# Kernel tuning notes

Hardware: AMD Instinct MI355X
Metric: run time of the kernel (lower is better)

## Reference

```python
import jax, jax.numpy as jnp
import numpy as np

B = 512
C = 256
HEADS = 16
DH = 16
SIGMA = 1e-4  # GaussianNoise(0.0001)
LEAK = 0.2


def _axial_attn(x, Wq, Wkv, Wo, bo, axis):
    # x: [B, 8, 4, 5, C]; attend along `axis`, folding other dims into batch.
    xm = jnp.moveaxis(x, axis, -2)                      # [..., T, C]
    q = xm @ Wq                                          # [..., T, C]
    kv = xm @ Wkv                                        # [..., T, 2C]
    k, v = kv[..., :C], kv[..., C:]
    hshape = q.shape[:-1] + (HEADS, DH)
    q = q.reshape(hshape)
    k = k.reshape(hshape)
    v = v.reshape(hshape)
    dots = jnp.einsum('...thd,...shd->...hts', q, k) * (DH ** -0.5)
    attn = jax.nn.softmax(dots, axis=-1)
    o = jnp.einsum('...hts,...shd->...thd', attn, v).reshape(xm.shape)
    o = o @ Wo + bo
    return jnp.moveaxis(o, -2, axis)


def setup_inputs() -> dict:
    key = jax.random.key(0)
    ks = jax.random.split(key, 12)
    inp = {
        'x': jax.random.normal(ks[0], (B, 8, 4, 5), jnp.float32),
        'noise': jax.random.normal(ks[1], (B, 8, 4, 5, 1), jnp.float32),
        'rand': jax.random.uniform(ks[2], (B, 8, 4, 5, 1), jnp.float32),
        # encoder Linear(2, 256, bias=False), stored as [in, out]
        'W_enc': jax.random.normal(ks[3], (2, C), jnp.float32) * (2 ** -0.5),
        # axial positional embedding (sum of per-axis params == one full param)
        'pos_emb': jax.random.normal(ks[4], (8, 4, 5, C), jnp.float32) * 0.02,
        # 2 AxialAttention layers x 3 axes of SelfAttention params
        'Wq': jax.random.normal(ks[5], (2, 3, C, C), jnp.float32) * (C ** -0.5),
        'Wkv': jax.random.normal(ks[6], (2, 3, C, 2 * C), jnp.float32) * (C ** -0.5),
        'Wo': jax.random.normal(ks[7], (2, 3, C, C), jnp.float32) * (C ** -0.5),
        'bo': jnp.zeros((2, 3, C), jnp.float32),
        # decoder Linear(256, 1, bias=True)
        'Wd': jax.random.normal(ks[8], (C, 1), jnp.float32) * (C ** -0.5),
        'bd': jnp.zeros((1,), jnp.float32),
    }
    return inp


def reference(x, noise, rand, W_enc, pos_emb, Wq, Wkv, Wo, bo, Wd, bd):
    h = x[..., None] + SIGMA * noise                  # unsqueeze + GaussianNoise
    h = jnp.concatenate([h, rand], axis=-1)           # [B,8,4,5,2]
    h = jnp.tanh(h @ W_enc)                           # [B,8,4,5,256]
    h = h + pos_emb                                   # axial positional embedding
    for l in range(2):                                # two AxialAttention blocks
        h = (_axial_attn(h, Wq[l, 0], Wkv[l, 0], Wo[l, 0], bo[l, 0], 1)
             + _axial_attn(h, Wq[l, 1], Wkv[l, 1], Wo[l, 1], bo[l, 1], 2)
             + _axial_attn(h, Wq[l, 2], Wkv[l, 2], Wo[l, 2], bo[l, 2], 3))
        h = jnp.where(h >= 0, h, LEAK * h)            # LeakyReLU(0.2)
    out = jax.nn.sigmoid(h @ Wd + bd)                 # decoder Linear + Sigmoid
    return out[..., 0]                                # squeeze(-1) -> [B,8,4,5]
```

## Files before the change

kernel.cpp:

```cpp
#include <hip/hip_runtime.h>
#include <hip/hip_bf16.h>
#include <math.h>

#define NPOS 81920
#define CDIM 256
#define SIGMA 1e-4f
#define LEAK 0.2f

typedef __hip_bfloat16 bf16;
typedef __bf16 bf16x8 __attribute__((ext_vector_type(8)));
typedef float f32x4 __attribute__((ext_vector_type(4)));

__device__ __forceinline__ float bf2f(unsigned short u) {
    return __uint_as_float(((unsigned)u) << 16);
}
__device__ __forceinline__ unsigned short f2bfu(float f) {
    bf16 h = __float2bfloat16(f);
    return *reinterpret_cast<unsigned short*>(&h);
}

__global__ void encode_kernel(const float* __restrict__ x, const float* __restrict__ noise,
                              const float* __restrict__ rnd, const float* __restrict__ We,
                              const float* __restrict__ pe, bf16* __restrict__ H) {
    int p = blockIdx.x;
    int c = threadIdx.x;
    float a = x[p] + SIGMA * noise[p];
    float b = rnd[p];
    float z = a * We[c] + b * We[CDIM + c];
    z = fminf(15.f, fmaxf(-15.f, z));
    float e = __expf(2.f * z);
    float th = 1.f - 2.f / (e + 1.f);
    H[(size_t)p * CDIM + c] = __float2bfloat16(th + pe[(p % 160) * CDIM + c]);
}

__global__ void bias3_kernel(const float* __restrict__ bo, float* __restrict__ bsum) {
    int l = blockIdx.x, c = threadIdx.x;
    bsum[l * CDIM + c] = bo[l * 768 + c] + bo[l * 768 + 256 + c] + bo[l * 768 + 512 + c];
}

__global__ void pack_qkv_kernel(const float* __restrict__ Wq, const float* __restrict__ Wkv,
                                bf16* __restrict__ out) {
    int mat = blockIdx.x / 768;
    int n = blockIdx.x % 768;
    int k = threadIdx.x;
    float v = (n < 256) ? Wq[(size_t)mat * 65536 + (size_t)k * 256 + n]
                        : Wkv[(size_t)mat * 131072 + (size_t)k * 512 + (n - 256)];
    out[(size_t)blockIdx.x * 256 + k] = __float2bfloat16(v);
}
__global__ void pack_wo_kernel(const float* __restrict__ Wo, bf16* __restrict__ out) {
    int l = blockIdx.x / 256;
    int n = blockIdx.x % 256;
    int ck = threadIdx.x;
    for (int a = 0; a < 3; a++)
        out[(size_t)(l * 256 + n) * 768 + a * 256 + ck] =
            __float2bfloat16(Wo[(((size_t)(l * 3 + a)) * 256 + ck) * 256 + n]);
}

__global__ __launch_bounds__(256, 2) void step_kernel(
    const bf16* __restrict__ Hg, const bf16* __restrict__ Wqkv, bf16* __restrict__ QKV,
    const bf16* __restrict__ O, const bf16* __restrict__ WoTl, bf16* __restrict__ Hnw,
    const float* __restrict__ bias, int nW, int nMblk) {
    __shared__ __bf16 smem[32768];
    int tid = threadIdx.x;
    int wave = tid >> 6, lane = tid & 63;
    int quad = lane >> 4, m = lane & 15;

    if (blockIdx.x >= nW) {
        __bf16* As = smem;
        __bf16* Bs = smem + 8192;
        int bid = blockIdx.x - nW;
        int xcd = bid & 7, slot = bid >> 3;
        int g = slot / 9;
        int nb = slot - g * 9;
        int mb = xcd + 8 * g;
        int bm = mb * 128, bn = nb * 256;
        int wr = (wave >> 1) * 64, wc = (wave & 1) * 128;
        f32x4 acc[4][8] = {};

#define STAGE_G(buf, k0)                                                                       \
    {                                                                                          \
        _Pragma("unroll") for (int rep = 0; rep < 2; rep++) {                                  \
            int ch = rep * 256 + wave * 64 + lane;                                             \
            int row = ch >> 2, cc = ch & 3, gc = cc ^ ((row >> 1) & 3);                        \
            __builtin_amdgcn_global_load_lds(                                                  \
                (const __attribute__((address_space(1))) void*)(Hg + (size_t)(bm + row) * CDIM \
                                                                + (k0) + gc * 8),              \
                (__attribute__((address_space(3))) void*)(As + (buf) * 4096                    \
                                                          + (rep * 256 + wave * 64) * 8),      \
                16, 0, 0);                                                                     \
        }                                                                                      \
        _Pragma("unroll") for (int rep = 0; rep < 4; rep++) {                                  \
            int ch = rep * 256 + wave * 64 + lane;                                             \
            int row = ch >> 2, cc = ch & 3, gc = cc ^ ((row >> 1) & 3);                        \
            __builtin_amdgcn_global_load_lds(                                                  \
                (const __attribute__((address_space(1))) void*)(Wqkv + (size_t)(bn + row) * 256\
                                                                + (k0) + gc * 8),              \
                (__attribute__((address_space(3))) void*)(Bs + (buf) * 8192                    \
                                                          + (rep * 256 + wave * 64) * 8),      \
                16, 0, 0);                                                                     \
        }                                                                                      \
    }

        STAGE_G(0, 0);
#pragma unroll
        for (int it = 0; it < 8; it++) {
            __syncthreads();
            if (it < 7) STAGE_G((it + 1) & 1, (it + 1) * 32);
            const __bf16* Ab = As + (it & 1) * 4096;
            const __bf16* Bb = Bs + (it & 1) * 8192;
            bf16x8 af[4], bfr[8];
#pragma unroll
            for (int i = 0; i < 4; i++) {
                int r = wr + i * 16 + m;
                af[i] = *(const bf16x8*)(Ab + r * 32 + ((quad ^ ((r >> 1) & 3)) * 8));
            }
#pragma unroll
            for (int j = 0; j < 8; j++) {
                int r = wc + j * 16 + m;
                bfr[j] = *(const bf16x8*)(Bb + r * 32 + ((quad ^ ((r >> 1) & 3)) * 8));
            }
#pragma unroll
            for (int i = 0; i < 4; i++)
#pragma unroll
                for (int j = 0; j < 8; j++)
                    acc[i][j] = __builtin_amdgcn_mfma_f32_16x16x32_bf16(af[i], bfr[j], acc[i][j], 0, 0, 0);
        }
#undef STAGE_G

#pragma unroll
        for (int i = 0; i < 4; i++)
#pragma unroll
            for (int j = 0; j < 8; j++)
#pragma unroll
                for (int r = 0; r < 4; r++) {
                    int row = bm + wr + i * 16 + quad * 4 + r;
                    int col = bn + wc + j * 16 + m;
                    QKV[(size_t)row * 2304 + col] = __float2bfloat16(acc[i][j][r]);
                }
    } else {
        __bf16* As = smem;
        __bf16* Bs = smem + 16384;
        int bid = blockIdx.x;
        int xcd = bid & 7, slot = bid >> 3;
        int g = slot >> 1;
        int nb = slot & 1;
        int mb = xcd + 8 * g;
        int bm = mb * 128, bn = nb * 128;
        int wr = (wave >> 1) * 64, wc = (wave & 1) * 64;
        f32x4 acc[4][4] = {};

#define STAGE_W(buf, k0)                                                                       \
    {                                                                                          \
        _Pragma("unroll") for (int rep = 0; rep < 4; rep++) {                                  \
            int ch = rep * 256 + wave * 64 + lane;                                             \
            int row = ch >> 3, cc = ch & 7, gc = cc ^ (row & 7);                               \
            __builtin_amdgcn_global_load_lds(                                                  \
                (const __attribute__((address_space(1))) void*)(O + (size_t)(bm + row) * 768   \
                                                                + (k0) + gc * 8),              \
                (__attribute__((address_space(3))) void*)(As + (buf) * 8192                    \
                                                          + (rep * 256 + wave * 64) * 8),      \
                16, 0, 0);                                                                     \
        }                                                                                      \
        _Pragma("unroll") for (int rep = 0; rep < 4; rep++) {                                  \
            int ch = rep * 256 + wave * 64 + lane;                                             \
            int row = ch >> 3, cc = ch & 7, gc = cc ^ (row & 7);                               \
            __builtin_amdgcn_global_load_lds(                                                  \
                (const __attribute__((address_space(1))) void*)(WoTl + (size_t)(bn + row) * 768\
                                                                + (k0) + gc * 8),              \
                (__attribute__((address_space(3))) void*)(Bs + (buf) * 8192                    \
                                                          + (rep * 256 + wave * 64) * 8),      \
                16, 0, 0);                                                                     \
        }                                                                                      \
    }

        STAGE_W(0, 0);
#pragma unroll
        for (int it = 0; it < 12; it++) {
            __syncthreads();
            if (it < 11) STAGE_W((it + 1) & 1, (it + 1) * 64);
            const __bf16* Ab = As + (it & 1) * 8192;
            const __bf16* Bb = Bs + (it & 1) * 8192;
#pragma unroll
            for (int kk = 0; kk < 2; kk++) {
                bf16x8 af[4], bfr[4];
#pragma unroll
                for (int i = 0; i < 4; i++) {
                    int r = wr + i * 16 + m, cix = kk * 4 + quad;
                    af[i] = *(const bf16x8*)(Ab + r * 64 + ((cix ^ (r & 7)) * 8));
                }
#pragma unroll
                for (int j = 0; j < 4; j++) {
                    int r = wc + j * 16 + m, cix = kk * 4 + quad;
                    bfr[j] = *(const bf16x8*)(Bb + r * 64 + ((cix ^ (r & 7)) * 8));
                }
#pragma unroll
                for (int i = 0; i < 4; i++)
#pragma unroll
                    for (int j = 0; j < 4; j++)
                        acc[i][j] = __builtin_amdgcn_mfma_f32_16x16x32_bf16(af[i], bfr[j], acc[i][j], 0, 0, 0);
            }
        }
#undef STAGE_W

#pragma unroll
        for (int i = 0; i < 4; i++)
#pragma unroll
            for (int j = 0; j < 4; j++)
#pragma unroll
                for (int r = 0; r < 4; r++) {
                    int row = bm + wr + i * 16 + quad * 4 + r;
                    int col = bn + wc + j * 16 + m;
                    float v = acc[i][j][r] + bias[col];
                    v = v >= 0.f ? v : LEAK * v;
                    Hnw[(size_t)row * CDIM + col] = __float2bfloat16(v);
                }
    }
}

template <int AXIS>
__device__ __forceinline__ void attn_axis(const bf16* __restrict__ QKV, bf16* __restrict__ O,
                                          int seq, int lane) {
    constexpr int T      = (AXIS == 0) ? 8 : (AXIS == 1) ? 4 : 5;
    constexpr int STRIDE = (AXIS == 0) ? 20 : (AXIS == 1) ? 5 : 1;
    int base;
    if (AXIS == 0)      { int b = seq / 20, r = seq % 20; base = b * 160 + r; }
    else if (AXIS == 1) { int b = seq / 40, r = seq % 40; base = b * 160 + (r / 5) * 20 + (r % 5); }
    else                { int b = seq / 32, r = seq % 32; base = b * 160 + r * 5; }

    float q[T][4], k[T][4], v[T][4];
#pragma unroll
    for (int t = 0; t < T; t++) {
        const unsigned short* rowp =
            (const unsigned short*)QKV + (size_t)(base + t * STRIDE) * 2304 + AXIS * 768 + lane * 4;
        ushort4 qu = *(const ushort4*)(rowp);
        ushort4 ku = *(const ushort4*)(rowp + 256);
        ushort4 vu = *(const ushort4*)(rowp + 512);
        q[t][0] = bf2f(qu.x); q[t][1] = bf2f(qu.y); q[t][2] = bf2f(qu.z); q[t][3] = bf2f(qu.w);
        k[t][0] = bf2f(ku.x); k[t][1] = bf2f(ku.y); k[t][2] = bf2f(ku.z); k[t][3] = bf2f(ku.w);
        v[t][0] = bf2f(vu.x); v[t][1] = bf2f(vu.y); v[t][2] = bf2f(vu.z); v[t][3] = bf2f(vu.w);
    }

#pragma unroll
    for (int t = 0; t < T; t++) {
        float sc[T];
#pragma unroll
        for (int s = 0; s < T; s++) {
            float p = q[t][0] * k[s][0] + q[t][1] * k[s][1] + q[t][2] * k[s][2] + q[t][3] * k[s][3];
            p += __shfl_xor(p, 1);
            p += __shfl_xor(p, 2);
            sc[s] = p * 0.25f;
        }
        float mx = sc[0];
#pragma unroll
        for (int s = 1; s < T; s++) mx = fmaxf(mx, sc[s]);
        float sum = 0.f;
#pragma unroll
        for (int s = 0; s < T; s++) { sc[s] = __expf(sc[s] - mx); sum += sc[s]; }
        float inv = 1.f / sum;
        float o0 = 0.f, o1 = 0.f, o2 = 0.f, o3 = 0.f;
#pragma unroll
        for (int s = 0; s < T; s++) {
            o0 += sc[s] * v[s][0]; o1 += sc[s] * v[s][1];
            o2 += sc[s] * v[s][2]; o3 += sc[s] * v[s][3];
        }
        ushort4 st;
        st.x = f2bfu(o0 * inv); st.y = f2bfu(o1 * inv);
        st.z = f2bfu(o2 * inv); st.w = f2bfu(o3 * inv);
        *(ushort4*)((unsigned short*)O + (size_t)(base + t * STRIDE) * 768 + AXIS * 256 + lane * 4) = st;
    }
}

__global__ __launch_bounds__(256) void attn_all(const bf16* __restrict__ QKV,
                                                bf16* __restrict__ O, int n0, int n1) {
    int wave = threadIdx.x >> 6, lane = threadIdx.x & 63;
    int blk = blockIdx.x;
    if (blk < n0)            attn_axis<0>(QKV, O, blk * 4 + wave, lane);
    else if (blk < n0 + n1)  attn_axis<1>(QKV, O, (blk - n0) * 4 + wave, lane);
    else                     attn_axis<2>(QKV, O, (blk - n0 - n1) * 4 + wave, lane);
}

__global__ void decode_kernel(const bf16* __restrict__ H, const float* __restrict__ Wd,
                              const float* __restrict__ bd, float* __restrict__ out) {
    int tid = threadIdx.x;
    int pos = blockIdx.x * 4 + (tid >> 6);
    int lane = tid & 63;
    float acc = 0.f;
#pragma unroll
    for (int q = 0; q < 4; q++) {
        int c = lane + q * 64;
        acc += __bfloat162float(H[(size_t)pos * CDIM + c]) * Wd[c];
    }
#pragma unroll
    for (int off = 32; off > 0; off >>= 1) acc += __shfl_down(acc, off);
    if (lane == 0) out[pos] = 1.f / (1.f + __expf(-(acc + bd[0])));
}

extern "C" void kernel_launch(void* const* d_in, const int* in_sizes, int n_in,
                              void* d_out, int out_size, void* d_ws, size_t ws_size,
                              hipStream_t stream) {
    const float* x     = (const float*)d_in[0];
    const float* noise = (const float*)d_in[1];
    const float* rnd   = (const float*)d_in[2];
    const float* We    = (const float*)d_in[3];
    const float* pe    = (const float*)d_in[4];
    const float* Wq    = (const float*)d_in[5];
    const float* Wkv   = (const float*)d_in[6];
    const float* Wo    = (const float*)d_in[7];
    const float* bo    = (const float*)d_in[8];
    const float* Wd    = (const float*)d_in[9];
    const float* bd    = (const float*)d_in[10];
    float* out = (float*)d_out;

    bf16* H0    = (bf16*)d_ws;
    bf16* H1    = H0 + (size_t)NPOS * CDIM;
    bf16* WqkvT = H1 + (size_t)NPOS * CDIM;
    bf16* WoT   = WqkvT + (size_t)2 * 2304 * 256;
    float* bsum = (float*)(WoT + (size_t)2 * 256 * 768);
    bf16* QKV   = (bf16*)(bsum + 512);

    size_t fixed = ((size_t)2 * NPOS * CDIM + (size_t)2 * 2304 * 256 + (size_t)2 * 256 * 768) * 2
                   + 512 * 4;
    int c = 4;
    while (c < 64 && fixed + (size_t)(NPOS / c) * (2304 + 768) * 2 > ws_size) c <<= 1;
    int mc = NPOS / c;
    bf16* O = QKV + (size_t)mc * 2304;
    bf16* Hbuf[3] = { H0, H1, H0 };

    pack_qkv_kernel<<<6 * 768, 256, 0, stream>>>(Wq, Wkv, WqkvT);
    pack_wo_kernel<<<2 * 256, 256, 0, stream>>>(Wo, WoT);
    bias3_kernel<<<2, 256, 0, stream>>>(bo, bsum);
    encode_kernel<<<NPOS, 256, 0, stream>>>(x, noise, rnd, We, pe, H0);

    int nMblk = mc / 128;
    int n0 = (mc / 160) * 20 / 4, n1 = (mc / 160) * 40 / 4, n2 = (mc / 160) * 32 / 4;
    int TT = 2 * c;

    for (int t = 0; t <= TT; t++) {
        int gG = (t < TT) ? nMblk * 9 : 0;
        int gW = (t >= 1) ? nMblk * 2 : 0;
        const bf16 *Hg = nullptr, *Wq_ = nullptr;
        if (gG) {
            int lg = t / c, cg = t % c;
            Hg = Hbuf[lg] + (size_t)cg * mc * CDIM;
            Wq_ = WqkvT + (size_t)lg * 2304 * 256;
        }
        const bf16* WoTl = nullptr; bf16* Hnw = nullptr; const float* bs = nullptr;
        if (gW) {
            int tw = t - 1, lw = tw / c, cw = tw % c;
            WoTl = WoT + (size_t)lw * 256 * 768;
            Hnw = Hbuf[lw + 1] + (size_t)cw * mc * CDIM;
            bs = bsum + lw * CDIM;
        }
        step_kernel<<<gG + gW, 256, 0, stream>>>(Hg, Wq_, QKV, O, WoTl, Hnw, bs, gW, nMblk);
        if (t < TT) attn_all<<<n0 + n1 + n2, 256, 0, stream>>>(QKV, O, n0, n1);
    }

    decode_kernel<<<NPOS / 4, 256, 0, stream>>>(Hbuf[2], Wd, bd, out);
}
```

Before: 674.8 us.

## Fuse attention into step kernel as a three-stage software pipeline with double buffers

Folds the separate attention launch into the step kernel, so each launch runs the QKV GEMM for chunk t, attention for chunk t-1 and the output-projection GEMM for chunk t-2 at the same time. Attention blocks are spread evenly through the grid. QKV and O buffers are double-buffered, and the minimum chunk count rises from 4 to 8 to fit the extra workspace. This halves the number of launches and removes the serialization between the GEMM and attention phases, but it uses smaller chunks and mixes block types with uneven cost. The attention blocks also reserve the GEMM's 64 KB of shared memory, which may hurt occupancy.

Result: slower. 777.6 us (+15.2%).

```diff
diff --git a/kernel.cpp b/kernel.cpp
--- a/kernel.cpp
+++ b/kernel.cpp
@@ -56,20 +56,88 @@
             __float2bfloat16(Wo[(((size_t)(l * 3 + a)) * 256 + ck) * 256 + n]);
 }
 
-__global__ __launch_bounds__(256, 2) void step_kernel(
-    const bf16* __restrict__ Hg, const bf16* __restrict__ Wqkv, bf16* __restrict__ QKV,
-    const bf16* __restrict__ O, const bf16* __restrict__ WoTl, bf16* __restrict__ Hnw,
-    const float* __restrict__ bias, int nW, int nMblk) {
+template <int AXIS>
+__device__ __forceinline__ void attn_axis(const bf16* __restrict__ QKV, bf16* __restrict__ O,
+                                          int seq, int lane) {
+    constexpr int T      = (AXIS == 0) ? 8 : (AXIS == 1) ? 4 : 5;
+    constexpr int STRIDE = (AXIS == 0) ? 20 : (AXIS == 1) ? 5 : 1;
+    int base;
+    if (AXIS == 0)      { int b = seq / 20, r = seq % 20; base = b * 160 + r; }
+    else if (AXIS == 1) { int b = seq / 40, r = seq % 40; base = b * 160 + (r / 5) * 20 + (r % 5); }
+    else                { int b = seq / 32, r = seq % 32; base = b * 160 + r * 5; }
+
+    float q[T][4], k[T][4], v[T][4];
+#pragma unroll
+    for (int t = 0; t < T; t++) {
+        const unsigned short* rowp =
+            (const unsigned short*)QKV + (size_t)(base + t * STRIDE) * 2304 + AXIS * 768 + lane * 4;
+        ushort4 qu = *(const ushort4*)(rowp);
+        ushort4 ku = *(const ushort4*)(rowp + 256);
+        ushort4 vu = *(const ushort4*)(rowp + 512);
+        q[t][0] = bf2f(qu.x); q[t][1] = bf2f(qu.y); q[t][2] = bf2f(qu.z); q[t][3] = bf2f(qu.w);
+        k[t][0] = bf2f(ku.x); k[t][1] = bf2f(ku.y); k[t][2] = bf2f(ku.z); k[t][3] = bf2f(ku.w);
+        v[t][0] = bf2f(vu.x); v[t][1] = bf2f(vu.y); v[t][2] = bf2f(vu.z); v[t][3] = bf2f(vu.w);
+    }
+
+#pragma unroll
+    for (int t = 0; t < T; t++) {
+        float sc[T];
+#pragma unroll
+        for (int s = 0; s < T; s++) {
+            float p = q[t][0] * k[s][0] + q[t][1] * k[s][1] + q[t][2] * k[s][2] + q[t][3] * k[s][3];
+            p += __shfl_xor(p, 1);
+            p += __shfl_xor(p, 2);
+            sc[s] = p * 0.25f;
+        }
+        float mx = sc[0];
+#pragma unroll
+        for (int s = 1; s < T; s++) mx = fmaxf(mx, sc[s]);
+        float sum = 0.f;
+#pragma unroll
+        for (int s = 0; s < T; s++) { sc[s] = __expf(sc[s] - mx); sum += sc[s]; }
+        float inv = 1.f / sum;
+        float o0 = 0.f, o1 = 0.f, o2 = 0.f, o3 = 0.f;
+#pragma unroll
+        for (int s = 0; s < T; s++) {
+            o0 += sc[s] * v[s][0]; o1 += sc[s] * v[s][1];
+            o2 += sc[s] * v[s][2]; o3 += sc[s] * v[s][3];
+        }
+        ushort4 st;
+        st.x = f2bfu(o0 * inv); st.y = f2bfu(o1 * inv);
+        st.z = f2bfu(o2 * inv); st.w = f2bfu(o3 * inv);
+        *(ushort4*)((unsigned short*)O + (size_t)(base + t * STRIDE) * 768 + AXIS * 256 + lane * 4) = st;
+    }
+}
+
+__global__ __launch_bounds__(256, 2) void step3_kernel(
+    const bf16* __restrict__ Hg, const bf16* __restrict__ Wqkv, bf16* __restrict__ QKVw,
+    const bf16* __restrict__ QKVr, bf16* __restrict__ Oa,
+    const bf16* __restrict__ Or, const bf16* __restrict__ WoTl, bf16* __restrict__ Hnw,
+    const float* __restrict__ bias,
+    int nA, int nW, int nT, int n0, int n1) {
     __shared__ __bf16 smem[32768];
     int tid = threadIdx.x;
     int wave = tid >> 6, lane = tid & 63;
     int quad = lane >> 4, m = lane & 15;
-
-    if (blockIdx.x >= nW) {
+    int bid = blockIdx.x;
+
+    long long p0 = (long long)bid * nA;
+    int aIdx = (int)(p0 / nT);
+    bool isA = ((p0 + nA) / nT) > aIdx;
+
+    if (isA) {
+        if (aIdx < n0)            attn_axis<0>(QKVr, Oa, aIdx * 4 + wave, lane);
+        else if (aIdx < n0 + n1)  attn_axis<1>(QKVr, Oa, (aIdx - n0) * 4 + wave, lane);
+        else                      attn_axis<2>(QKVr, Oa, (aIdx - n0 - n1) * 4 + wave, lane);
+        return;
+    }
+    int gw = bid - aIdx;
+
+    if (gw >= nW) {
         __bf16* As = smem;
         __bf16* Bs = smem + 8192;
-        int bid = blockIdx.x - nW;
-        int xcd = bid & 7, slot = bid >> 3;
+        int gb = gw - nW;
+        int xcd = gb & 7, slot = gb >> 3;
         int g = slot / 9;
         int nb = slot - g * 9;
         int mb = xcd + 8 * g;
@@ -135,13 +203,13 @@
                 for (int r = 0; r < 4; r++) {
                     int row = bm + wr + i * 16 + quad * 4 + r;
                     int col = bn + wc + j * 16 + m;
-                    QKV[(size_t)row * 2304 + col] = __float2bfloat16(acc[i][j][r]);
+                    QKVw[(size_t)row * 2304 + col] = __float2bfloat16(acc[i][j][r]);
                 }
     } else {
         __bf16* As = smem;
         __bf16* Bs = smem + 16384;
-        int bid = blockIdx.x;
-        int xcd = bid & 7, slot = bid >> 3;
+        int wb = gw;
+        int xcd = wb & 7, slot = wb >> 3;
         int g = slot >> 1;
         int nb = slot & 1;
         int mb = xcd + 8 * g;
@@ -155,7 +223,7 @@
             int ch = rep * 256 + wave * 64 + lane;                                             \
             int row = ch >> 3, cc = ch & 7, gc = cc ^ (row & 7);                               \
             __builtin_amdgcn_global_load_lds(                                                  \
-                (const __attribute__((address_space(1))) void*)(O + (size_t)(bm + row) * 768   \
+                (const __attribute__((address_space(1))) void*)(Or + (size_t)(bm + row) * 768  \
                                                                 + (k0) + gc * 8),              \
                 (__attribute__((address_space(3))) void*)(As + (buf) * 8192                    \
                                                           + (rep * 256 + wave * 64) * 8),      \
@@ -217,68 +285,6 @@
     }
 }
 
-template <int AXIS>
-__device__ __forceinline__ void attn_axis(const bf16* __restrict__ QKV, bf16* __restrict__ O,
-                                          int seq, int lane) {
-    constexpr int T      = (AXIS == 0) ? 8 : (AXIS == 1) ? 4 : 5;
-    constexpr int STRIDE = (AXIS == 0) ? 20 : (AXIS == 1) ? 5 : 1;
-    int base;
-    if (AXIS == 0)      { int b = seq / 20, r = seq % 20; base = b * 160 + r; }
-    else if (AXIS == 1) { int b = seq / 40, r = seq % 40; base = b * 160 + (r / 5) * 20 + (r % 5); }
-    else                { int b = seq / 32, r = seq % 32; base = b * 160 + r * 5; }
-
-    float q[T][4], k[T][4], v[T][4];
-#pragma unroll
-    for (int t = 0; t < T; t++) {
-        const unsigned short* rowp =
-            (const unsigned short*)QKV + (size_t)(base + t * STRIDE) * 2304 + AXIS * 768 + lane * 4;
-        ushort4 qu = *(const ushort4*)(rowp);
-        ushort4 ku = *(const ushort4*)(rowp + 256);
-        ushort4 vu = *(const ushort4*)(rowp + 512);
-        q[t][0] = bf2f(qu.x); q[t][1] = bf2f(qu.y); q[t][2] = bf2f(qu.z); q[t][3] = bf2f(qu.w);
-        k[t][0] = bf2f(ku.x); k[t][1] = bf2f(ku.y); k[t][2] = bf2f(ku.z); k[t][3] = bf2f(ku.w);
-        v[t][0] = bf2f(vu.x); v[t][1] = bf2f(vu.y); v[t][2] = bf2f(vu.z); v[t][3] = bf2f(vu.w);
-    }
-
-#pragma unroll
-    for (int t = 0; t < T; t++) {
-        float sc[T];
-#pragma unroll
-        for (int s = 0; s < T; s++) {
-            float p = q[t][0] * k[s][0] + q[t][1] * k[s][1] + q[t][2] * k[s][2] + q[t][3] * k[s][3];
-            p += __shfl_xor(p, 1);
-            p += __shfl_xor(p, 2);
-            sc[s] = p * 0.25f;
-        }
-        float mx = sc[0];
-#pragma unroll
-        for (int s = 1; s < T; s++) mx = fmaxf(mx, sc[s]);
-        float sum = 0.f;
-#pragma unroll
-        for (int s = 0; s < T; s++) { sc[s] = __expf(sc[s] - mx); sum += sc[s]; }
-        float inv = 1.f / sum;
-        float o0 = 0.f, o1 = 0.f, o2 = 0.f, o3 = 0.f;
-#pragma unroll
-        for (int s = 0; s < T; s++) {
-            o0 += sc[s] * v[s][0]; o1 += sc[s] * v[s][1];
-            o2 += sc[s] * v[s][2]; o3 += sc[s] * v[s][3];
-        }
-        ushort4 st;
-        st.x = f2bfu(o0 * inv); st.y = f2bfu(o1 * inv);
-        st.z = f2bfu(o2 * inv); st.w = f2bfu(o3 * inv);
-        *(ushort4*)((unsigned short*)O + (size_t)(base + t * STRIDE) * 768 + AXIS * 256 + lane * 4) = st;
-    }
-}
-
-__global__ __launch_bounds__(256) void attn_all(const bf16* __restrict__ QKV,
-                                                bf16* __restrict__ O, int n0, int n1) {
-    int wave = threadIdx.x >> 6, lane = threadIdx.x & 63;
-    int blk = blockIdx.x;
-    if (blk < n0)            attn_axis<0>(QKV, O, blk * 4 + wave, lane);
-    else if (blk < n0 + n1)  attn_axis<1>(QKV, O, (blk - n0) * 4 + wave, lane);
-    else                     attn_axis<2>(QKV, O, (blk - n0 - n1) * 4 + wave, lane);
-}
-
 __global__ void decode_kernel(const bf16* __restrict__ H, const float* __restrict__ Wd,
                               const float* __restrict__ bd, float* __restrict__ out) {
     int tid = threadIdx.x;
@@ -316,14 +322,16 @@
     bf16* WqkvT = H1 + (size_t)NPOS * CDIM;
     bf16* WoT   = WqkvT + (size_t)2 * 2304 * 256;
     float* bsum = (float*)(WoT + (size_t)2 * 256 * 768);
-    bf16* QKV   = (bf16*)(bsum + 512);
+    bf16* bufs  = (bf16*)(bsum + 512);
 
     size_t fixed = ((size_t)2 * NPOS * CDIM + (size_t)2 * 2304 * 256 + (size_t)2 * 256 * 768) * 2
                    + 512 * 4;
-    int c = 4;
-    while (c < 64 && fixed + (size_t)(NPOS / c) * (2304 + 768) * 2 > ws_size) c <<= 1;
+    int c = 8;
+    while (c < 64 && fixed + (size_t)(NPOS / c) * 2 * (2304 + 768) * 2 > ws_size) c <<= 1;
     int mc = NPOS / c;
-    bf16* O = QKV + (size_t)mc * 2304;
+    bf16* QKVb[2] = { bufs, bufs + (size_t)mc * 2304 };
+    bf16* Ob[2]   = { bufs + (size_t)2 * mc * 2304,
+                      bufs + (size_t)2 * mc * 2304 + (size_t)mc * 768 };
     bf16* Hbuf[3] = { H0, H1, H0 };
 
     pack_qkv_kernel<<<6 * 768, 256, 0, stream>>>(Wq, Wkv, WqkvT);
@@ -333,26 +341,33 @@
 
     int nMblk = mc / 128;
     int n0 = (mc / 160) * 20 / 4, n1 = (mc / 160) * 40 / 4, n2 = (mc / 160) * 32 / 4;
+    int nAfull = n0 + n1 + n2;
     int TT = 2 * c;
 
-    for (int t = 0; t <= TT; t++) {
+    for (int t = 0; t <= TT + 1; t++) {
         int gG = (t < TT) ? nMblk * 9 : 0;
-        int gW = (t >= 1) ? nMblk * 2 : 0;
-        const bf16 *Hg = nullptr, *Wq_ = nullptr;
+        int gA = (t >= 1 && t <= TT) ? nAfull : 0;
+        int gW = (t >= 2) ? nMblk * 2 : 0;
+        const bf16 *Hg = nullptr, *Wq_ = nullptr; bf16* QKVw = nullptr;
         if (gG) {
             int lg = t / c, cg = t % c;
             Hg = Hbuf[lg] + (size_t)cg * mc * CDIM;
             Wq_ = WqkvT + (size_t)lg * 2304 * 256;
-        }
-        const bf16* WoTl = nullptr; bf16* Hnw = nullptr; const float* bs = nullptr;
+            QKVw = QKVb[t & 1];
+        }
+        const bf16* QKVr = nullptr; bf16* Oa = nullptr;
+        if (gA) { QKVr = QKVb[(t - 1) & 1]; Oa = Ob[(t - 1) & 1]; }
+        const bf16 *Or = nullptr, *WoTl = nullptr; bf16* Hnw = nullptr; const float* bs = nullptr;
         if (gW) {
-            int tw = t - 1, lw = tw / c, cw = tw % c;
+            int tw = t - 2, lw = tw / c, cw = tw % c;
+            Or = Ob[tw & 1];
             WoTl = WoT + (size_t)lw * 256 * 768;
             Hnw = Hbuf[lw + 1] + (size_t)cw * mc * CDIM;
             bs = bsum + lw * CDIM;
         }
-        step_kernel<<<gG + gW, 256, 0, stream>>>(Hg, Wq_, QKV, O, WoTl, Hnw, bs, gW, nMblk);
-        if (t < TT) attn_all<<<n0 + n1 + n2, 256, 0, stream>>>(QKV, O, n0, n1);
+        int nT = gG + gA + gW;
+        step3_kernel<<<nT, 256, 0, stream>>>(Hg, Wq_, QKVw, QKVr, Oa, Or, WoTl, Hnw, bs,
+                                             gA, gW, nT, n0, n1);
     }
 
     decode_kernel<<<NPOS / 4, 256, 0, stream>>>(Hbuf[2], Wd, bd, out);
```
